# Performance work log

Measured on AMD Instinct MI355X. Metric: run time of the kernel, lower is better.

Reference implementation:

```python
import jax, jax.numpy as jnp
import numpy as np

NUM_SLOTS = 16
CORE_INPUT_SIZE = 256


def _perm_matrix(key):
    p = jax.random.permutation(key, NUM_SLOTS)
    return jnp.eye(NUM_SLOTS, dtype=jnp.float32)[p]


def setup_inputs() -> dict:
    key = jax.random.key(0)
    kx, k1, k2 = jax.random.split(key, 3)
    x = jax.random.normal(kx, (512, 16, 16, CORE_INPUT_SIZE), dtype=jnp.float32)
    Ppos = _perm_matrix(k1)
    Pneg = _perm_matrix(k2)
    return {"x": x, "Ppos": Ppos, "Pneg": Pneg}


def reference(x, Ppos, Pneg):
    B, O, I, C = x.shape
    # split last dim into (num_slots rows, cols)
    xr = x.reshape(B, O, I, NUM_SLOTS, C // NUM_SLOTS)
    # permutation-matrix einsum on the slots axis (a one-hot gather)
    xpos = jnp.einsum('ij,boijk->boiik'.replace('boij', 'bOIj').replace('boii', 'bOIi'), Ppos, xr) if False else jnp.einsum('ij,...jk->...ik', Ppos, xr)
    xneg = jnp.einsum('ij,...jk->...ik', Pneg, xr)
    return (xpos - xneg).reshape(B, O, I, C)
```

## Files before the change

### kernel.cpp

```cpp
#include <hip/hip_runtime.h>


#define NSLOTS 16

typedef float fvec4 __attribute__((ext_vector_type(4)));

__global__ __launch_bounds__(256, 8) void permute_ws_kernel(
    const fvec4* __restrict__ x,
    const float* __restrict__ Ppos,
    const float* __restrict__ Pneg,
    fvec4* __restrict__ out,
    int total_v4)
{
    __shared__ int soff_p[NSLOTS];
    __shared__ int soff_n[NSLOTS];

    const int t = threadIdx.x;
    if (t < NSLOTS) {
        int ip = 0, in_ = 0;
        #pragma unroll
        for (int j = 0; j < NSLOTS; ++j) {
            if (Ppos[t * NSLOTS + j] > 0.5f) ip = j;
            if (Pneg[t * NSLOTS + j] > 0.5f) in_ = j;
        }
        soff_p[t] = ip << 2;
        soff_n[t] = in_ << 2;
    }
    __syncthreads();

    const int idx    = blockIdx.x * blockDim.x + threadIdx.x;
    const int stride = gridDim.x * blockDim.x;

    const int v    = idx & 63;
    const int slot = v >> 2;
    const int k4   = v & 3;
    const int dp = soff_p[slot] + k4 - v;
    const int dn = soff_n[slot] + k4 - v;

    int i = idx;
    for (; i + 3 * stride < total_v4; i += 4 * stride) {
        const fvec4 a0 = x[i              + dp];
        const fvec4 b0 = x[i              + dn];
        const fvec4 a1 = x[i +     stride + dp];
        const fvec4 b1 = x[i +     stride + dn];
        const fvec4 a2 = x[i + 2 * stride + dp];
        const fvec4 b2 = x[i + 2 * stride + dn];
        const fvec4 a3 = x[i + 3 * stride + dp];
        const fvec4 b3 = x[i + 3 * stride + dn];
        out[i             ] = a0 - b0;
        out[i +     stride] = a1 - b1;
        out[i + 2 * stride] = a2 - b2;
        out[i + 3 * stride] = a3 - b3;
    }
    for (; i < total_v4; i += stride) {
        const fvec4 a = x[i + dp];
        const fvec4 b = x[i + dn];
        out[i] = a - b;
    }
}

extern "C" void kernel_launch(void* const* d_in, const int* in_sizes, int n_in,
                              void* d_out, int out_size, void* d_ws, size_t ws_size,
                              hipStream_t stream)
{
    const fvec4* x    = (const fvec4*)d_in[0];
    const float* Ppos = (const float*)d_in[1];
    const float* Pneg = (const float*)d_in[2];
    fvec4*       out  = (fvec4*)d_out;

    const int total_v4 = out_size / 4;

    const int block = 256;
    int blocks_needed = (total_v4 + block - 1) / block;
    int grid = blocks_needed > 2048 ? 2048 : blocks_needed;

    permute_ws_kernel<<<grid, block, 0, stream>>>(x, Ppos, Pneg, out, total_v4);
}
```

Baseline: 239.8 us.

## Replace grid-stride loop with one-shot blocks covering 1024 vec4 each

Drops the capped 2048-block grid-stride loop and launches enough blocks that each thread handles exactly four vec4 outputs at fixed 256-element offsets. This is meant to raise the number of resident waves and memory requests in flight and remove loop overhead. In exchange, every block repeats the small permutation-table setup and barrier, and many more blocks are launched.

```diff
diff --git a/kernel.cpp b/kernel.cpp
--- a/kernel.cpp
+++ b/kernel.cpp
@@ -28,34 +28,37 @@
     }
     __syncthreads();
 
-    const int idx    = blockIdx.x * blockDim.x + threadIdx.x;
-    const int stride = gridDim.x * blockDim.x;
-
-    const int v    = idx & 63;
+    const int v    = t & 63;
     const int slot = v >> 2;
     const int k4   = v & 3;
     const int dp = soff_p[slot] + k4 - v;
     const int dn = soff_n[slot] + k4 - v;
 
-    int i = idx;
-    for (; i + 3 * stride < total_v4; i += 4 * stride) {
-        const fvec4 a0 = x[i              + dp];
-        const fvec4 b0 = x[i              + dn];
-        const fvec4 a1 = x[i +     stride + dp];
-        const fvec4 b1 = x[i +     stride + dn];
-        const fvec4 a2 = x[i + 2 * stride + dp];
-        const fvec4 b2 = x[i + 2 * stride + dn];
-        const fvec4 a3 = x[i + 3 * stride + dp];
-        const fvec4 b3 = x[i + 3 * stride + dn];
-        out[i             ] = a0 - b0;
-        out[i +     stride] = a1 - b1;
-        out[i + 2 * stride] = a2 - b2;
-        out[i + 3 * stride] = a3 - b3;
-    }
-    for (; i < total_v4; i += stride) {
-        const fvec4 a = x[i + dp];
-        const fvec4 b = x[i + dn];
-        out[i] = a - b;
+    const int i0 = blockIdx.x * 1024 + t;
+
+    if (i0 + 768 < total_v4) {
+        const fvec4 a0 = x[i0 +   0 + dp];
+        const fvec4 b0 = x[i0 +   0 + dn];
+        const fvec4 a1 = x[i0 + 256 + dp];
+        const fvec4 b1 = x[i0 + 256 + dn];
+        const fvec4 a2 = x[i0 + 512 + dp];
+        const fvec4 b2 = x[i0 + 512 + dn];
+        const fvec4 a3 = x[i0 + 768 + dp];
+        const fvec4 b3 = x[i0 + 768 + dn];
+        out[i0 +   0] = a0 - b0;
+        out[i0 + 256] = a1 - b1;
+        out[i0 + 512] = a2 - b2;
+        out[i0 + 768] = a3 - b3;
+    } else {
+        #pragma unroll
+        for (int j = 0; j < 4; ++j) {
+            const int i = i0 + 256 * j;
+            if (i < total_v4) {
+                const fvec4 a = x[i + dp];
+                const fvec4 b = x[i + dn];
+                out[i] = a - b;
+            }
+        }
     }
 }
 
@@ -71,8 +74,7 @@
     const int total_v4 = out_size / 4;
 
     const int block = 256;
-    int blocks_needed = (total_v4 + block - 1) / block;
-    int grid = blocks_needed > 2048 ? 2048 : blocks_needed;
+    const int grid = (total_v4 + 1023) / 1024;
 
     permute_ws_kernel<<<grid, block, 0, stream>>>(x, Ppos, Pneg, out, total_v4);
 }
```

Measured after the change: 231.0 us. 1.04x faster.
